# Performance work log

Measured on AMD Instinct MI355X. Metric: run time of the kernel, lower is better.

The kernel has to match this reference:

```python
import jax, jax.numpy as jnp
import numpy as np

SIGMA = 1.0

def _pairwise_sqdist(x, y):
    # x: [N,3], y: [M,3] -> [N,M] squared distances via gram expansion
    xx = jnp.sum(x * x, axis=-1)[:, None]
    yy = jnp.sum(y * y, axis=-1)[None, :]
    xy = x @ y.T
    return jnp.maximum(xx + yy - 2.0 * xy, 0.0)

def _cauchy(d2, sigma):
    return 1.0 / (1.0 + d2 / (sigma * sigma))

def setup_inputs() -> dict:
    key = jax.random.key(0)
    k1, k2, k3, k4 = jax.random.split(key, 4)
    V, N, M = 4096, 8192, 8192
    src_vertices = jax.random.normal(k1, (V, 3), dtype=jnp.float32)
    tar_normals = jax.random.normal(k2, (M, 3), dtype=jnp.float32)
    tar_centers = jax.random.normal(k3, (M, 3), dtype=jnp.float32)
    src_indices = jax.random.randint(k4, (N, 3), 0, V)
    return {"src_vertices": src_vertices, "tar_normals": tar_normals,
            "tar_centers": tar_centers, "src_indices": src_indices}

def reference(src_vertices, tar_normals, tar_centers, src_indices):
    # Gather triangle vertices: [N,3(verts),3(xyz)]
    tris = src_vertices[src_indices]
    a, b, c = tris[:, 0, :], tris[:, 1, :], tris[:, 2, :]
    normals = 0.5 * jnp.cross(a - b, c - b)        # [N,3]
    centers = tris.sum(axis=1) / 3.0               # [N,3]

    # Currents energy with cauchy kernel K(x,y) = 1/(1 + |x-y|^2/sigma^2)
    K_ss = _cauchy(_pairwise_sqdist(centers, centers), SIGMA)      # [N,N]
    K_st = _cauchy(_pairwise_sqdist(centers, tar_centers), SIGMA)  # [N,M]
    K_tt = _cauchy(_pairwise_sqdist(tar_centers, tar_centers), SIGMA)  # [M,M]

    e_ss = jnp.sum(K_ss * (normals @ normals.T))
    e_st = jnp.sum(K_st * (normals @ tar_normals.T))
    e_tt = jnp.sum(K_tt * (tar_normals @ tar_normals.T))
    return e_ss - 2.0 * e_st + e_tt
```

## Files before the change

kernel.cpp:

```cpp
#include <hip/hip_runtime.h>

typedef short bf16x8 __attribute__((ext_vector_type(8)));
typedef float f32x16 __attribute__((ext_vector_type(16)));

static __device__ __forceinline__ unsigned short f2bf(float x) {
    unsigned u = __builtin_bit_cast(unsigned, x);
    unsigned r = (u + 0x7FFFu + ((u >> 16) & 1u)) >> 16;
    return (unsigned short)r;
}
static __device__ __forceinline__ float bf2f(unsigned short h) {
    unsigned u = (unsigned)h << 16;
    return __builtin_bit_cast(float, u);
}


__global__ void dc_pack(const float* __restrict__ verts,
                        const float* __restrict__ tnorm,
                        const float* __restrict__ tcent,
                        const int* __restrict__ idx,
                        unsigned short* __restrict__ ws,
                        float* __restrict__ out,
                        int N, int M) {
    int p = blockIdx.x * blockDim.x + threadIdx.x;
    if (p == 0) out[0] = 0.0f;
    int P = N + M;
    if (p >= P) return;

    float cx, cy, cz, nx, ny, nz;
    if (p < N) {
        int i0 = idx[3 * p + 0], i1 = idx[3 * p + 1], i2 = idx[3 * p + 2];
        float ax = verts[3 * i0], ay = verts[3 * i0 + 1], az = verts[3 * i0 + 2];
        float bx = verts[3 * i1], by = verts[3 * i1 + 1], bz = verts[3 * i1 + 2];
        float qx = verts[3 * i2], qy = verts[3 * i2 + 1], qz = verts[3 * i2 + 2];
        float ux = ax - bx, uy = ay - by, uz = az - bz;
        float vx = qx - bx, vy = qy - by, vz = qz - bz;
        nx = 0.5f * (uy * vz - uz * vy);
        ny = 0.5f * (uz * vx - ux * vz);
        nz = 0.5f * (ux * vy - uy * vx);
        cx = (ax + bx + qx) * (1.0f / 3.0f);
        cy = (ay + by + qy) * (1.0f / 3.0f);
        cz = (az + bz + qz) * (1.0f / 3.0f);
    } else {
        int t = p - N;
        cx = tcent[3 * t]; cy = tcent[3 * t + 1]; cz = tcent[3 * t + 2];
        nx = -tnorm[3 * t]; ny = -tnorm[3 * t + 1]; nz = -tnorm[3 * t + 2];
    }

    unsigned short chx = f2bf(cx), chy = f2bf(cy), chz = f2bf(cz);
    unsigned short clx = f2bf(cx - bf2f(chx));
    unsigned short cly = f2bf(cy - bf2f(chy));
    unsigned short clz = f2bf(cz - bf2f(chz));
    unsigned short nhx = f2bf(nx), nhy = f2bf(ny), nhz = f2bf(nz);
    unsigned short nlx = f2bf(nx - bf2f(nhx));
    unsigned short nly = f2bf(ny - bf2f(nhy));
    unsigned short nlz = f2bf(nz - bf2f(nhz));
    float ex = bf2f(chx) + bf2f(clx);
    float ey = bf2f(chy) + bf2f(cly);
    float ez = bf2f(chz) + bf2f(clz);
    float s = ex * ex + ey * ey + ez * ez;
    unsigned short sh = f2bf(s), sl = f2bf(s - bf2f(sh));
    unsigned short m2hx = f2bf(-2.0f * bf2f(chx)), m2hy = f2bf(-2.0f * bf2f(chy)), m2hz = f2bf(-2.0f * bf2f(chz));
    unsigned short m2lx = f2bf(-2.0f * bf2f(clx)), m2ly = f2bf(-2.0f * bf2f(cly)), m2lz = f2bf(-2.0f * bf2f(clz));
    const unsigned short one = 0x3F80;

    __align__(16) unsigned short A1v[16] = {
        m2hx, m2hy, m2hz,  m2hx, m2hy, m2hz,  m2lx, m2ly, m2lz,
        sh, sl,  one, one,  one,  0, 0 };
    __align__(16) unsigned short B1v[16] = {
        chx, chy, chz,  clx, cly, clz,  chx, chy, chz,
        one, one,  sh, sl,  one,  0, 0 };
    __align__(16) unsigned short A2v[16] = {
        nhx, nhy, nhz,  nhx, nhy, nhz,  nlx, nly, nlz,
        0, 0, 0, 0, 0, 0, 0 };
    __align__(16) unsigned short B2v[16] = {
        nhx, nhy, nhz,  nlx, nly, nlz,  nhx, nhy, nhz,
        0, 0, 0, 0, 0, 0, 0 };

    size_t arr = (size_t)P * 16;
    unsigned short* A1 = ws;
    unsigned short* A2 = ws + arr;
    unsigned short* B1 = ws + 2 * arr;
    unsigned short* B2 = ws + 3 * arr;

    int tile = p >> 5, m = p & 31;
    size_t lo = ((size_t)tile * 64 + m) * 8;
    size_t hi = lo + 32 * 8;

    *(uint4*)(A1 + lo) = *(const uint4*)&A1v[0];
    *(uint4*)(A1 + hi) = *(const uint4*)&A1v[8];
    *(uint4*)(A2 + lo) = *(const uint4*)&A2v[0];
    *(uint4*)(A2 + hi) = *(const uint4*)&A2v[8];
    *(uint4*)(B1 + lo) = *(const uint4*)&B1v[0];
    *(uint4*)(B1 + hi) = *(const uint4*)&B1v[8];
    *(uint4*)(B2 + lo) = *(const uint4*)&B2v[0];
    *(uint4*)(B2 + hi) = *(const uint4*)&B2v[8];
}

static __device__ __forceinline__ void acc4(float4& part, const f32x16& d1, const f32x16& d2) {
#pragma unroll
    for (int g = 0; g < 4; ++g) {
        const int r = 4 * g;
        float p01 = d1[r] * d1[r + 1];
        float p23 = d1[r + 2] * d1[r + 3];
        float n01 = fmaf(d2[r], d1[r + 1], d2[r + 1] * d1[r]);
        float n23 = fmaf(d2[r + 2], d1[r + 3], d2[r + 3] * d1[r + 2]);
        float t   = p01 * p23;
        float num = fmaf(n01, p23, n23 * p01);
        (&part.x)[g] = fmaf(num, __builtin_amdgcn_rcpf(t), (&part.x)[g]);
    }
}

__global__ __launch_bounds__(256, 4) void dc_pair_mfma(
    const unsigned short* __restrict__ ws, float* __restrict__ out, int P) {
    __shared__ float wsum[4];

    const int nT = P >> 5;
    size_t arr = (size_t)P * 16;
    const unsigned short* A1 = ws;
    const unsigned short* A2 = ws + arr;
    const unsigned short* B1 = ws + 2 * arr;
    const unsigned short* B2 = ws + 3 * arr;

    int tid = threadIdx.x;
    int lane = tid & 63, wv = tid >> 6;
    int gi = blockIdx.x * 4 + wv;
    int rp = gi >> 4, c = gi & 15;
    int I0 = 2 * rp, I1 = I0 + 1;

    const size_t lo = (size_t)lane * 8;

    bf16x8 a1_0 = *(const bf16x8*)(A1 + (size_t)I0 * 512 + lo);
    bf16x8 a2_0 = *(const bf16x8*)(A2 + (size_t)I0 * 512 + lo);
    bf16x8 a1_1 = *(const bf16x8*)(A1 + (size_t)I1 * 512 + lo);
    bf16x8 a2_1 = *(const bf16x8*)(A2 + (size_t)I1 * 512 + lo);

    const f32x16 zero = {0.f,0.f,0.f,0.f,0.f,0.f,0.f,0.f,0.f,0.f,0.f,0.f,0.f,0.f,0.f,0.f};
    float4 partA = make_float4(0.f, 0.f, 0.f, 0.f);
    float4 corrP = make_float4(0.f, 0.f, 0.f, 0.f);
    float4 corrM = make_float4(0.f, 0.f, 0.f, 0.f);

    auto wrap = [&](int j) -> size_t {
        return (size_t)(j >= nT ? j - nT : j) * 512;
    };
    auto process = [&](const bf16x8& b1, const bf16x8& b2) {
        f32x16 d1 = __builtin_amdgcn_mfma_f32_32x32x16_bf16(a1_0, b1, zero, 0, 0, 0);
        f32x16 d2 = __builtin_amdgcn_mfma_f32_32x32x16_bf16(a2_0, b2, zero, 0, 0, 0);
        f32x16 e1 = __builtin_amdgcn_mfma_f32_32x32x16_bf16(a1_1, b1, zero, 0, 0, 0);
        f32x16 e2 = __builtin_amdgcn_mfma_f32_32x32x16_bf16(a2_1, b2, zero, 0, 0, 0);
        acc4(partA, d1, d2);
        acc4(partA, e1, e2);
    };
    auto one_tile = [&](float4& part, const bf16x8& x1, const bf16x8& x2, int jm) {
        const bf16x8 b1 = *(const bf16x8*)(B1 + (size_t)jm * 512 + lo);
        const bf16x8 b2 = *(const bf16x8*)(B2 + (size_t)jm * 512 + lo);
        f32x16 d1 = __builtin_amdgcn_mfma_f32_32x32x16_bf16(x1, b1, zero, 0, 0, 0);
        f32x16 d2 = __builtin_amdgcn_mfma_f32_32x32x16_bf16(x2, b2, zero, 0, 0, 0);
        acc4(part, d1, d2);
    };

    int js = I0 + 1 + 16 * c;

    bf16x8 bA1 = *(const bf16x8*)(B1 + wrap(js) + lo);
    bf16x8 bA2 = *(const bf16x8*)(B2 + wrap(js) + lo);
#pragma unroll 1
    for (int it = 0; it < 16; it += 2) {
        size_t o1 = wrap(js + it + 1);
        bf16x8 bB1 = *(const bf16x8*)(B1 + o1 + lo);
        bf16x8 bB2 = *(const bf16x8*)(B2 + o1 + lo);
        process(bA1, bA2);
        size_t o2 = wrap(js + it + 2);
        bA1 = *(const bf16x8*)(B1 + o2 + lo);
        bA2 = *(const bf16x8*)(B2 + o2 + lo);
        process(bB1, bB2);
    }

    if (c == 0) {
        one_tile(corrP, a1_0, a2_0, I0);
        one_tile(corrM, a1_1, a2_1, I0 + 1);
    } else if (c == 15) {
        int v = I0 + 256; if (v >= nT) v -= nT;
        int y = I0 + 257; if (y >= nT) y -= nT;
        one_tile(corrM, a1_0, a2_0, v);
        one_tile(corrP, a1_1, a2_1, y);
    }

    float s = 2.0f * (partA.x + partA.y + partA.z + partA.w)
            + (corrP.x + corrP.y + corrP.z + corrP.w)
            - (corrM.x + corrM.y + corrM.z + corrM.w);
#pragma unroll
    for (int off = 32; off > 0; off >>= 1) s += __shfl_down(s, off, 64);
    if (lane == 0) wsum[wv] = s;
    __syncthreads();
    if (tid == 0) {
        float t = wsum[0] + wsum[1] + wsum[2] + wsum[3];
        atomicAdd(out, t);
    }
}

extern "C" void kernel_launch(void* const* d_in, const int* in_sizes, int n_in,
                              void* d_out, int out_size, void* d_ws, size_t ws_size,
                              hipStream_t stream) {
    const float* verts = (const float*)d_in[0];
    const float* tnorm = (const float*)d_in[1];
    const float* tcent = (const float*)d_in[2];
    const int*   sidx  = (const int*)d_in[3];

    int M = in_sizes[1] / 3;
    int N = in_sizes[3] / 3;
    int P = N + M;

    unsigned short* ws = (unsigned short*)d_ws;
    float* out = (float*)d_out;

    int bblocks = (P + 255) / 256;
    dc_pack<<<bblocks, 256, 0, stream>>>(verts, tnorm, tcent, sidx, ws, out, N, M);

    dc_pair_mfma<<<1024, 256, 0, stream>>>(ws, out, P);
}
```

Baseline: 83.47 us.

## Batch eight kernel terms per reciprocal and enlarge pair-kernel blocks to 1024 threads

```diff
diff --git a/kernel.cpp b/kernel.cpp
--- a/kernel.cpp
+++ b/kernel.cpp
@@ -21,7 +21,7 @@
                         unsigned short* __restrict__ ws,
                         float* __restrict__ out,
                         int N, int M) {
-    int p = blockIdx.x * blockDim.x + threadIdx.x;
+    int p = blockIdx.x * 64 + threadIdx.x;
     if (p == 0) out[0] = 0.0f;
     int P = N + M;
     if (p >= P) return;
@@ -96,23 +96,31 @@
     *(uint4*)(B2 + hi) = *(const uint4*)&B2v[8];
 }
 
-static __device__ __forceinline__ void acc4(float4& part, const f32x16& d1, const f32x16& d2) {
+static __device__ __forceinline__ void acc8(float4& part, const f32x16& d1, const f32x16& d2) {
 #pragma unroll
-    for (int g = 0; g < 4; ++g) {
-        const int r = 4 * g;
-        float p01 = d1[r] * d1[r + 1];
+    for (int g = 0; g < 2; ++g) {
+        const int r = 8 * g;
+        float p01 = d1[r + 0] * d1[r + 1];
         float p23 = d1[r + 2] * d1[r + 3];
-        float n01 = fmaf(d2[r], d1[r + 1], d2[r + 1] * d1[r]);
+        float p45 = d1[r + 4] * d1[r + 5];
+        float p67 = d1[r + 6] * d1[r + 7];
+        float n01 = fmaf(d2[r + 0], d1[r + 1], d2[r + 1] * d1[r + 0]);
         float n23 = fmaf(d2[r + 2], d1[r + 3], d2[r + 3] * d1[r + 2]);
-        float t   = p01 * p23;
-        float num = fmaf(n01, p23, n23 * p01);
-        (&part.x)[g] = fmaf(num, __builtin_amdgcn_rcpf(t), (&part.x)[g]);
-    }
-}
-
-__global__ __launch_bounds__(256, 4) void dc_pair_mfma(
+        float n45 = fmaf(d2[r + 4], d1[r + 5], d2[r + 5] * d1[r + 4]);
+        float n67 = fmaf(d2[r + 6], d1[r + 7], d2[r + 7] * d1[r + 6]);
+        float q03 = p01 * p23;
+        float q47 = p45 * p67;
+        float m03 = fmaf(n01, p23, n23 * p01);
+        float m47 = fmaf(n45, p67, n67 * p45);
+        float T   = q03 * q47;
+        float NUM = fmaf(m03, q47, m47 * q03);
+        (&part.x)[g] = fmaf(NUM, __builtin_amdgcn_rcpf(T), (&part.x)[g]);
+    }
+}
+
+__global__ __launch_bounds__(1024, 4) void dc_pair_mfma(
     const unsigned short* __restrict__ ws, float* __restrict__ out, int P) {
-    __shared__ float wsum[4];
+    __shared__ float wsum[16];
 
     const int nT = P >> 5;
     size_t arr = (size_t)P * 16;
@@ -123,7 +131,7 @@
 
     int tid = threadIdx.x;
     int lane = tid & 63, wv = tid >> 6;
-    int gi = blockIdx.x * 4 + wv;
+    int gi = blockIdx.x * 16 + wv;
     int rp = gi >> 4, c = gi & 15;
     int I0 = 2 * rp, I1 = I0 + 1;
 
@@ -147,15 +155,15 @@
         f32x16 d2 = __builtin_amdgcn_mfma_f32_32x32x16_bf16(a2_0, b2, zero, 0, 0, 0);
         f32x16 e1 = __builtin_amdgcn_mfma_f32_32x32x16_bf16(a1_1, b1, zero, 0, 0, 0);
         f32x16 e2 = __builtin_amdgcn_mfma_f32_32x32x16_bf16(a2_1, b2, zero, 0, 0, 0);
-        acc4(partA, d1, d2);
-        acc4(partA, e1, e2);
+        acc8(partA, d1, d2);
+        acc8(partA, e1, e2);
     };
     auto one_tile = [&](float4& part, const bf16x8& x1, const bf16x8& x2, int jm) {
         const bf16x8 b1 = *(const bf16x8*)(B1 + (size_t)jm * 512 + lo);
         const bf16x8 b2 = *(const bf16x8*)(B2 + (size_t)jm * 512 + lo);
         f32x16 d1 = __builtin_amdgcn_mfma_f32_32x32x16_bf16(x1, b1, zero, 0, 0, 0);
         f32x16 d2 = __builtin_amdgcn_mfma_f32_32x32x16_bf16(x2, b2, zero, 0, 0, 0);
-        acc4(part, d1, d2);
+        acc8(part, d1, d2);
     };
 
     int js = I0 + 1 + 16 * c;
@@ -192,7 +200,9 @@
     if (lane == 0) wsum[wv] = s;
     __syncthreads();
     if (tid == 0) {
-        float t = wsum[0] + wsum[1] + wsum[2] + wsum[3];
+        float t = 0.f;
+#pragma unroll
+        for (int i = 0; i < 16; ++i) t += wsum[i];
         atomicAdd(out, t);
     }
 }
@@ -212,8 +222,8 @@
     unsigned short* ws = (unsigned short*)d_ws;
     float* out = (float*)d_out;
 
-    int bblocks = (P + 255) / 256;
-    dc_pack<<<bblocks, 256, 0, stream>>>(verts, tnorm, tcent, sidx, ws, out, N, M);
-
-    dc_pair_mfma<<<1024, 256, 0, stream>>>(ws, out, P);
-}
+    int pblocks = (P + 63) / 64;
+    dc_pack<<<pblocks, 64, 0, stream>>>(verts, tnorm, tcent, sidx, ws, out, N, M);
+
+    dc_pair_mfma<<<256, 1024, 0, stream>>>(ws, out, P);
+}
```

After: 80.03 us. 1.04x faster.
